# Kernel optimization log

Measured on AMD Instinct MI355X. Metric: run time of the kernel, lower is better.

The kernel has to match this reference:

```python
import jax, jax.numpy as jnp
import numpy as np

D_STATE = 16


def setup_inputs() -> dict:
    key = jax.random.key(0)
    ks = jax.random.split(key, 7)
    B, S, D = 8, 4096, 64
    ds = D_STATE
    x = jax.random.normal(ks[0], (B, S, D), dtype=jnp.float32)
    # Selection layers modeled as Linear(d_model, out). W_A scaled small so the
    # random transition matrices are contractive over 4096 steps.
    W_A = jax.random.normal(ks[1], (D, ds * ds), dtype=jnp.float32) * 0.01
    b_A = jnp.zeros((ds * ds,), dtype=jnp.float32)
    W_B = jax.random.normal(ks[2], (D, ds * D), dtype=jnp.float32) * 0.05
    b_B = jnp.zeros((ds * D,), dtype=jnp.float32)
    W_C = jax.random.normal(ks[3], (D, ds * D), dtype=jnp.float32) * 0.05
    b_C = jnp.zeros((ds * D,), dtype=jnp.float32)
    return {"x": x, "W_A": W_A, "b_A": b_A, "W_B": W_B, "b_B": b_B,
            "W_C": W_C, "b_C": b_C}


def reference(x, W_A, b_A, W_B, b_B, W_C, b_C):
    B, S, D = x.shape
    ds = D_STATE
    # Input-dependent (selective) parameters per timestep
    A = (x @ W_A + b_A).reshape(B, S, ds, ds)      # [B,S,ds,ds]
    Bm = (x @ W_B + b_B).reshape(B, S, ds, D)      # [B,S,ds,D]
    Cm = (x @ W_C + b_C).reshape(B, S, ds, D)      # [B,S,ds,D]
    # Pre-contract B_t @ x_t once: [B,S,ds]
    Bx = jnp.einsum('bsnd,bsd->bsn', Bm, x)

    def step(h, inputs):
        A_t, Bx_t = inputs                          # [B,ds,ds], [B,ds]
        h = jnp.einsum('bij,bj->bi', A_t, h) + Bx_t
        return h, h

    h0 = jnp.zeros((B, ds), dtype=x.dtype)
    _, hs = jax.lax.scan(step, h0,
                         (jnp.swapaxes(A, 0, 1), jnp.swapaxes(Bx, 0, 1)))
    hs = jnp.swapaxes(hs, 0, 1)                     # [B,S,ds]
    # output_t = C_t^T @ h_t  -> [B,S,D]
    return jnp.einsum('bsnd,bsn->bsd', Cm, hs)
```

## Files before the change

### kernel.cpp

```cpp
#include <hip/hip_runtime.h>

#define BATCH   8
#define SEQ     4096
#define DM      64
#define DS      16
#define BS      (BATCH*SEQ)
#define CHUNK   16
#define NCHT    (BS/CHUNK)
#define SG      16
#define NSG     (NCHT/SG)

typedef __attribute__((ext_vector_type(8))) __bf16 bf16x8;
typedef __attribute__((ext_vector_type(4))) float  f32x4;

__device__ __forceinline__ unsigned short f2bf(float f) {
  unsigned int u = __float_as_uint(f);
  u += 0x7fffu + ((u >> 16) & 1u);
  return (unsigned short)(u >> 16);
}
__device__ __forceinline__ float bflo(unsigned int u) { return __uint_as_float(u << 16); }
__device__ __forceinline__ float bfhi(unsigned int u) { return __uint_as_float(u & 0xffff0000u); }

#define AS_I 20
#define AS_T 324

__global__ __launch_bounds__(256) void k0_castw(
    const float* __restrict__ WA, const float* __restrict__ WB,
    const float* __restrict__ WC,
    unsigned short* __restrict__ WAt, unsigned short* __restrict__ WBt,
    unsigned short* __restrict__ WCt)
{
  const int o = blockIdx.x * 256 + threadIdx.x;
  if (o < 16384) {
    const int c = o >> 6, e = o & 63;
    WAt[o] = f2bf(WA[e * 256 + c]);
  } else if (o < 16384 + 65536) {
    const int p = o - 16384;
    const int c = p >> 6, e = p & 63;
    WBt[p] = f2bf(WB[e * 1024 + c]);
  } else {
    const int p = o - 16384 - 65536;
    const int c = p >> 6, e = p & 63;
    WCt[p] = f2bf(WC[e * 1024 + c]);
  }
}

__global__ __launch_bounds__(128) void g1(
    const float* __restrict__ x, const unsigned short* __restrict__ WBt,
    const float* __restrict__ bB, const unsigned short* __restrict__ WAt,
    const float* __restrict__ bA, unsigned short* __restrict__ xb,
    unsigned short* __restrict__ Wt_ws, float* __restrict__ u_ws,
    float* __restrict__ P_ws, float* __restrict__ v_ws)
{
  __shared__ __align__(16) unsigned char smem[32 * AS_T * 2];
  float (*xs)[68]     = (float (*)[68])smem;
  float* bBs          = (float*)(smem + 8704);
  unsigned short* As  = (unsigned short*)smem;
  __shared__ __align__(16) float bxs[32][16];
  __shared__ __align__(16) float us[2][16];

  const int tid  = threadIdx.x;
  const int lane = tid & 63;
  const int l15  = lane & 15;
  const int quad = lane >> 4;
  const int w    = tid >> 6;
  const int t0   = blockIdx.x * 32;
  const int twl  = w * 16;

  {
    const float4* xg = (const float4*)(x + (size_t)t0 * DM);
    #pragma unroll
    for (int i = 0; i < 4; ++i) {
      const int f4 = tid + 128 * i;
      ((float4*)&xs[f4 >> 4][0])[f4 & 15] = xg[f4];
    }
    ((float4*)bBs)[tid]       = ((const float4*)bB)[tid];
    ((float4*)bBs)[tid + 128] = ((const float4*)bB)[tid + 128];
    if (tid < 32) us[tid >> 4][tid & 15] = 0.f;
  }
  __syncthreads();

  bf16x8 a0, a1;
  {
    const int row = twl + l15;
    union { bf16x8 v; ushort4 s[2]; } ua, ub;
    float4 p0 = *(const float4*)&xs[row][quad * 8];
    float4 p1 = *(const float4*)&xs[row][quad * 8 + 4];
    float4 p2 = *(const float4*)&xs[row][32 + quad * 8];
    float4 p3 = *(const float4*)&xs[row][32 + quad * 8 + 4];
    ua.s[0] = (ushort4){f2bf(p0.x), f2bf(p0.y), f2bf(p0.z), f2bf(p0.w)};
    ua.s[1] = (ushort4){f2bf(p1.x), f2bf(p1.y), f2bf(p1.z), f2bf(p1.w)};
    ub.s[0] = (ushort4){f2bf(p2.x), f2bf(p2.y), f2bf(p2.z), f2bf(p2.w)};
    ub.s[1] = (ushort4){f2bf(p3.x), f2bf(p3.y), f2bf(p3.z), f2bf(p3.w)};
    a0 = ua.v; a1 = ub.v;
    unsigned short* xp = xb + (size_t)(t0 + row) * 64 + quad * 8;
    *(bf16x8*)xp        = a0;
    *(bf16x8*)(xp + 32) = a1;
  }

  #pragma unroll 2
  for (int n = 0; n < 16; ++n) {
    f32x4 ac[4];
    #pragma unroll
    for (int r = 0; r < 4; ++r) {
      const bf16x8* wv = (const bf16x8*)(WBt + (size_t)((n * 4 + r) * 16 + l15) * 64);
      f32x4 t = {0.f, 0.f, 0.f, 0.f};
      t = __builtin_amdgcn_mfma_f32_16x16x32_bf16(a0, wv[quad],     t, 0, 0, 0);
      t = __builtin_amdgcn_mfma_f32_16x16x32_bf16(a1, wv[quad + 4], t, 0, 0, 0);
      ac[r] = t;
    }
    float part[4] = {0.f, 0.f, 0.f, 0.f};
    #pragma unroll
    for (int r = 0; r < 4; ++r) {
      const float bb = bBs[n * 64 + r * 16 + l15];
      #pragma unroll
      for (int reg = 0; reg < 4; ++reg) {
        const int tl = twl + quad * 4 + reg;
        part[reg] = fmaf(ac[r][reg] + bb, xs[tl][r * 16 + l15], part[reg]);
      }
    }
    #pragma unroll
    for (int off = 1; off < 16; off <<= 1) {
      #pragma unroll
      for (int reg = 0; reg < 4; ++reg)
        part[reg] += __shfl_xor(part[reg], off, 64);
    }
    if (l15 == 0) {
      #pragma unroll
      for (int reg = 0; reg < 4; ++reg)
        bxs[twl + quad * 4 + reg][n] = part[reg];
    }
  }
  __syncthreads();

  #pragma unroll 2
  for (int ns = 0; ns < 16; ++ns) {
    const bf16x8* wv = (const bf16x8*)(WAt + (size_t)(ns * 16 + l15) * 64);
    f32x4 acc = {0.f, 0.f, 0.f, 0.f};
    acc = __builtin_amdgcn_mfma_f32_16x16x32_bf16(a0, wv[quad],     acc, 0, 0, 0);
    acc = __builtin_amdgcn_mfma_f32_16x16x32_bf16(a1, wv[quad + 4], acc, 0, 0, 0);
    const float bias = bA[ns * 16 + l15];
    #pragma unroll
    for (int r = 0; r < 4; ++r)
      As[(twl + quad * 4 + r) * AS_T + ns * AS_I + l15] = f2bf(acc[r] + bias);
  }
  __syncthreads();

  {
    bf16x8 wb;
    #pragma unroll
    for (int j = 0; j < 8; ++j) wb[j] = (__bf16)((quad * 8 + j == l15) ? 1.f : 0.f);
    f32x4 d = {0.f, 0.f, 0.f, 0.f};
    const int qq = quad & 1;

    #pragma unroll 1
    for (int t = 0; t < CHUNK; ++t) {
      const int tl = twl + t;
      const unsigned short* rp = &As[tl * AS_T + l15 * AS_I];
      uint2 r0 = *(const uint2*)(rp);
      uint2 r1 = *(const uint2*)(rp + 4);
      uint2 r2 = *(const uint2*)(rp + 8);
      uint2 r3 = *(const uint2*)(rp + 12);

      uint4 abits;
      if (quad == 0)      abits = make_uint4(r0.x, r0.y, r1.x, r1.y);
      else if (quad == 1) abits = make_uint4(r2.x, r2.y, r3.x, r3.y);
      else                abits = make_uint4(0u, 0u, 0u, 0u);
      bf16x8 af = *(bf16x8*)&abits;

      f32x4 z4 = {0.f, 0.f, 0.f, 0.f};
      d = __builtin_amdgcn_mfma_f32_16x16x32_bf16(af, wb, z4, 0, 0, 0);

      float nu = bxs[tl][l15];
      {
        float4 U0 = *(const float4*)&us[w][0];
        float4 U1 = *(const float4*)&us[w][4];
        float4 U2 = *(const float4*)&us[w][8];
        float4 U3 = *(const float4*)&us[w][12];
        nu = fmaf(bflo(r0.x), U0.x, nu); nu = fmaf(bfhi(r0.x), U0.y, nu);
        nu = fmaf(bflo(r0.y), U0.z, nu); nu = fmaf(bfhi(r0.y), U0.w, nu);
        nu = fmaf(bflo(r1.x), U1.x, nu); nu = fmaf(bfhi(r1.x), U1.y, nu);
        nu = fmaf(bflo(r1.y), U1.z, nu); nu = fmaf(bfhi(r1.y), U1.w, nu);
        nu = fmaf(bflo(r2.x), U2.x, nu); nu = fmaf(bfhi(r2.x), U2.y, nu);
        nu = fmaf(bflo(r2.y), U2.z, nu); nu = fmaf(bfhi(r2.y), U2.w, nu);
        nu = fmaf(bflo(r3.x), U3.x, nu); nu = fmaf(bfhi(r3.x), U3.y, nu);
        nu = fmaf(bflo(r3.y), U3.z, nu); nu = fmaf(bfhi(r3.y), U3.w, nu);
      }

      bf16x8 nb;
      nb[0] = (__bf16)__shfl(d[0], (2 * qq + 0) * 16 + l15, 64);
      nb[1] = (__bf16)__shfl(d[1], (2 * qq + 0) * 16 + l15, 64);
      nb[2] = (__bf16)__shfl(d[2], (2 * qq + 0) * 16 + l15, 64);
      nb[3] = (__bf16)__shfl(d[3], (2 * qq + 0) * 16 + l15, 64);
      nb[4] = (__bf16)__shfl(d[0], (2 * qq + 1) * 16 + l15, 64);
      nb[5] = (__bf16)__shfl(d[1], (2 * qq + 1) * 16 + l15, 64);
      nb[6] = (__bf16)__shfl(d[2], (2 * qq + 1) * 16 + l15, 64);
      nb[7] = (__bf16)__shfl(d[3], (2 * qq + 1) * 16 + l15, 64);
      wb = nb;

      if (quad == 0) {
        us[w][l15] = nu;
        bxs[tl][l15] = nu;
      }
      #pragma unroll
      for (int r = 0; r < 4; ++r)
        As[tl * AS_T + (quad * 4 + r) * AS_I + l15] = f2bf(d[r]);
    }

    const int chunk = blockIdx.x * 2 + w;
    #pragma unroll
    for (int r = 0; r < 4; ++r)
      P_ws[(size_t)chunk * 256 + (quad * 4 + r) * 16 + l15] = d[r];
    if (quad == 0) v_ws[(size_t)chunk * DS + l15] = us[w][l15];
  }
  __syncthreads();

  {
    uint4* Wg = (uint4*)(Wt_ws + (size_t)t0 * 256);
    #pragma unroll 1
    for (int z = 0; z < 8; ++z) {
      const int p4 = z * 128 + tid;
      const int f  = p4 * 8;
      const int t  = f >> 8, i = (f >> 4) & 15, k = f & 15;
      const unsigned short* sp = &As[t * AS_T + i * AS_I + k];
      uint2 lo = *(const uint2*)(sp);
      uint2 hi = *(const uint2*)(sp + 4);
      Wg[p4] = make_uint4(lo.x, lo.y, hi.x, hi.y);
    }
    ((float4*)(u_ws + (size_t)t0 * DS))[tid] = ((const float4*)&bxs[0][0])[tid];
  }
}

__global__ __launch_bounds__(256) void k3a(
    const float* __restrict__ P_ws, const float* __restrict__ v_ws,
    float* __restrict__ Q_ws, float* __restrict__ w_ws)
{
  __shared__ float wsv[4][16];
  const int tid  = threadIdx.x;
  const int lane = tid & 63;
  const int l15  = lane & 15;
  const int quad = lane >> 4;
  const int wv   = tid >> 6;
  const int s    = blockIdx.x * 4 + wv;
  const int qq   = quad & 1;

  if (lane < 16) wsv[wv][lane] = 0.f;
  bf16x8 wb;
  #pragma unroll
  for (int j = 0; j < 8; ++j) wb[j] = (__bf16)((quad * 8 + j == l15) ? 1.f : 0.f);
  f32x4 d = {0.f, 0.f, 0.f, 0.f};

  #pragma unroll 1
  for (int t = 0; t < SG; ++t) {
    const int chunk = s * SG + t;
    float4 p0 = {0.f,0.f,0.f,0.f}, p1 = {0.f,0.f,0.f,0.f};
    if (quad < 2) {
      const float4* pr = (const float4*)(P_ws + (size_t)chunk * 256 + l15 * 16 + quad * 8);
      p0 = pr[0]; p1 = pr[1];
    }
    bf16x8 af;
    af[0] = (__bf16)p0.x; af[1] = (__bf16)p0.y; af[2] = (__bf16)p0.z; af[3] = (__bf16)p0.w;
    af[4] = (__bf16)p1.x; af[5] = (__bf16)p1.y; af[6] = (__bf16)p1.z; af[7] = (__bf16)p1.w;

    f32x4 z4 = {0.f, 0.f, 0.f, 0.f};
    d = __builtin_amdgcn_mfma_f32_16x16x32_bf16(af, wb, z4, 0, 0, 0);

    float part = 0.f;
    if (quad < 2) {
      const float* wrow = &wsv[wv][quad * 8];
      part = p0.x*wrow[0] + p0.y*wrow[1] + p0.z*wrow[2] + p0.w*wrow[3]
           + p1.x*wrow[4] + p1.y*wrow[5] + p1.z*wrow[6] + p1.w*wrow[7];
    }
    part += __shfl_xor(part, 16, 64);
    const float nv = v_ws[(size_t)chunk * DS + l15];

    bf16x8 nb;
    nb[0] = (__bf16)__shfl(d[0], (2 * qq + 0) * 16 + l15, 64);
    nb[1] = (__bf16)__shfl(d[1], (2 * qq + 0) * 16 + l15, 64);
    nb[2] = (__bf16)__shfl(d[2], (2 * qq + 0) * 16 + l15, 64);
    nb[3] = (__bf16)__shfl(d[3], (2 * qq + 0) * 16 + l15, 64);
    nb[4] = (__bf16)__shfl(d[0], (2 * qq + 1) * 16 + l15, 64);
    nb[5] = (__bf16)__shfl(d[1], (2 * qq + 1) * 16 + l15, 64);
    nb[6] = (__bf16)__shfl(d[2], (2 * qq + 1) * 16 + l15, 64);
    nb[7] = (__bf16)__shfl(d[3], (2 * qq + 1) * 16 + l15, 64);
    wb = nb;

    if (quad == 0) wsv[wv][l15] = part + nv;
  }

  #pragma unroll
  for (int r = 0; r < 4; ++r)
    Q_ws[(size_t)s * 256 + (quad * 4 + r) * 16 + l15] = d[r];
  if (quad == 0) w_ws[(size_t)s * DS + l15] = wsv[wv][l15];
}

__global__ __launch_bounds__(128) void k3b(
    const float* __restrict__ Q_ws, const float* __restrict__ w_ws,
    float* __restrict__ hbg_ws)
{
  const int tid = threadIdx.x;
  const int b = tid >> 4;
  const int r = tid & 15;
  float h = 0.f;

  #pragma unroll 1
  for (int g = 0; g < 16; ++g) {
    const int s = b * 16 + g;
    const float4* Pr = (const float4*)&Q_ws[(size_t)s * 256 + r * 16];
    float4 c0 = Pr[0], c1 = Pr[1], c2 = Pr[2], c3 = Pr[3];
    const float vc = w_ws[(size_t)s * DS + r];
    hbg_ws[(size_t)s * DS + r] = h;
    float acc = vc;
    acc += c0.x*__shfl(h, 0,16) + c0.y*__shfl(h, 1,16) + c0.z*__shfl(h, 2,16) + c0.w*__shfl(h, 3,16);
    acc += c1.x*__shfl(h, 4,16) + c1.y*__shfl(h, 5,16) + c1.z*__shfl(h, 6,16) + c1.w*__shfl(h, 7,16);
    acc += c2.x*__shfl(h, 8,16) + c2.y*__shfl(h, 9,16) + c2.z*__shfl(h,10,16) + c2.w*__shfl(h,11,16);
    acc += c3.x*__shfl(h,12,16) + c3.y*__shfl(h,13,16) + c3.z*__shfl(h,14,16) + c3.w*__shfl(h,15,16);
    h = acc;
  }
}

__global__ __launch_bounds__(256) void k3c(
    const float* __restrict__ P_ws, const float* __restrict__ v_ws,
    const float* __restrict__ hbg_ws, float* __restrict__ hb_ws)
{
  const int tid = threadIdx.x;
  const int s = blockIdx.x * 16 + (tid >> 4);
  const int r = tid & 15;
  float h = hbg_ws[(size_t)s * DS + r];

  #pragma unroll 1
  for (int t = 0; t < SG; ++t) {
    const int chunk = s * SG + t;
    const float4* Pr = (const float4*)&P_ws[(size_t)chunk * 256 + r * 16];
    float4 c0 = Pr[0], c1 = Pr[1], c2 = Pr[2], c3 = Pr[3];
    const float vc = v_ws[(size_t)chunk * DS + r];
    hb_ws[(size_t)chunk * DS + r] = h;
    float acc = vc;
    acc += c0.x*__shfl(h, 0,16) + c0.y*__shfl(h, 1,16) + c0.z*__shfl(h, 2,16) + c0.w*__shfl(h, 3,16);
    acc += c1.x*__shfl(h, 4,16) + c1.y*__shfl(h, 5,16) + c1.z*__shfl(h, 6,16) + c1.w*__shfl(h, 7,16);
    acc += c2.x*__shfl(h, 8,16) + c2.y*__shfl(h, 9,16) + c2.z*__shfl(h,10,16) + c2.w*__shfl(h,11,16);
    acc += c3.x*__shfl(h,12,16) + c3.y*__shfl(h,13,16) + c3.z*__shfl(h,14,16) + c3.w*__shfl(h,15,16);
    h = acc;
  }
}

__global__ __launch_bounds__(256) void g2(
    const unsigned short* __restrict__ xb, const unsigned short* __restrict__ WCt,
    const float* __restrict__ bC, const unsigned short* __restrict__ Wt_ws,
    const float* __restrict__ u_ws, const float* __restrict__ hb_ws,
    float* __restrict__ out)
{
  __shared__ float hsh[64][17];
  __shared__ float bCs[1024];
  const int tid  = threadIdx.x;
  const int lane = tid & 63;
  const int l15  = lane & 15;
  const int quad = lane >> 4;
  const int w    = tid >> 6;
  const int t0   = blockIdx.x * 64;
  const int twl  = w * 16;

  ((float4*)bCs)[tid] = ((const float4*)bC)[tid];

  #pragma unroll
  for (int z = 0; z < 4; ++z) {
    const int gcell = z * 256 + tid;
    const int tl = gcell >> 4, i = gcell & 15;
    const int t = t0 + tl;
    const uint4* wr = (const uint4*)(Wt_ws + (size_t)t * 256 + i * 16);
    uint4 wa = wr[0], wbv = wr[1];
    const float4* hp = (const float4*)(hb_ws + (size_t)(t >> 4) * DS);
    float4 h0 = hp[0], h1 = hp[1], h2 = hp[2], h3 = hp[3];
    float acc = u_ws[(size_t)t * DS + i];
    acc = fmaf(bflo(wa.x),  h0.x, acc); acc = fmaf(bfhi(wa.x),  h0.y, acc);
    acc = fmaf(bflo(wa.y),  h0.z, acc); acc = fmaf(bfhi(wa.y),  h0.w, acc);
    acc = fmaf(bflo(wa.z),  h1.x, acc); acc = fmaf(bfhi(wa.z),  h1.y, acc);
    acc = fmaf(bflo(wa.w),  h1.z, acc); acc = fmaf(bfhi(wa.w),  h1.w, acc);
    acc = fmaf(bflo(wbv.x), h2.x, acc); acc = fmaf(bfhi(wbv.x), h2.y, acc);
    acc = fmaf(bflo(wbv.y), h2.z, acc); acc = fmaf(bfhi(wbv.y), h2.w, acc);
    acc = fmaf(bflo(wbv.z), h3.x, acc); acc = fmaf(bfhi(wbv.z), h3.y, acc);
    acc = fmaf(bflo(wbv.w), h3.z, acc); acc = fmaf(bfhi(wbv.w), h3.w, acc);
    hsh[tl][i] = acc;
  }

  const bf16x8* xv = (const bf16x8*)(xb + (size_t)(t0 + twl + l15) * 64);
  bf16x8 a0 = xv[quad];
  bf16x8 a1 = xv[quad + 4];
  __syncthreads();

  f32x4 ota[4];
  #pragma unroll
  for (int r = 0; r < 4; ++r) ota[r] = (f32x4){0.f, 0.f, 0.f, 0.f};

  #pragma unroll 2
  for (int n = 0; n < 16; ++n) {
    f32x4 ac[4];
    #pragma unroll
    for (int r = 0; r < 4; ++r) {
      const bf16x8* wv = (const bf16x8*)(WCt + (size_t)((n * 4 + r) * 16 + l15) * 64);
      f32x4 t = {0.f, 0.f, 0.f, 0.f};
      t = __builtin_amdgcn_mfma_f32_16x16x32_bf16(a0, wv[quad],     t, 0, 0, 0);
      t = __builtin_amdgcn_mfma_f32_16x16x32_bf16(a1, wv[quad + 4], t, 0, 0, 0);
      ac[r] = t;
    }
    float hn[4];
    #pragma unroll
    for (int reg = 0; reg < 4; ++reg) hn[reg] = hsh[twl + quad * 4 + reg][n];
    #pragma unroll
    for (int r = 0; r < 4; ++r) {
      const float bc = bCs[n * 64 + r * 16 + l15];
      #pragma unroll
      for (int reg = 0; reg < 4; ++reg)
        ota[r][reg] = fmaf(ac[r][reg] + bc, hn[reg], ota[r][reg]);
    }
  }

  #pragma unroll
  for (int r = 0; r < 4; ++r)
    #pragma unroll
    for (int reg = 0; reg < 4; ++reg)
      out[(size_t)(t0 + twl + quad * 4 + reg) * DM + r * 16 + l15] = ota[r][reg];
}

extern "C" void kernel_launch(void* const* d_in, const int* in_sizes, int n_in,
                              void* d_out, int out_size, void* d_ws, size_t ws_size,
                              hipStream_t stream) {
  const float* x  = (const float*)d_in[0];
  const float* WA = (const float*)d_in[1];
  const float* bA = (const float*)d_in[2];
  const float* WB = (const float*)d_in[3];
  const float* bB = (const float*)d_in[4];
  const float* WC = (const float*)d_in[5];
  const float* bC = (const float*)d_in[6];
  float* out = (float*)d_out;

  float* ws     = (float*)d_ws;
  float* P_ws   = ws;
  float* v_ws   = P_ws   + (size_t)NCHT * 256;
  float* u_ws   = v_ws   + (size_t)NCHT * DS;
  float* Q_ws   = u_ws   + (size_t)BS * DS;
  float* w_ws   = Q_ws   + (size_t)NSG * 256;
  float* hbg_ws = w_ws   + (size_t)NSG * DS;
  float* hb_ws  = hbg_ws + (size_t)NSG * DS;
  unsigned short* xb    = (unsigned short*)(hb_ws + (size_t)NCHT * DS);
  unsigned short* WAt   = xb  + (size_t)BS * 64;
  unsigned short* WBt   = WAt + 256 * 64;
  unsigned short* WCt   = WBt + 1024 * 64;
  unsigned short* Wt_ws = WCt + 1024 * 64;

  k0_castw<<<576,      256, 0, stream>>>(WA, WB, WC, WAt, WBt, WCt);
  g1      <<<BS / 32,  128, 0, stream>>>(x, WBt, bB, WAt, bA, xb, Wt_ws, u_ws, P_ws, v_ws);
  k3a     <<<NSG / 4,  256, 0, stream>>>(P_ws, v_ws, Q_ws, w_ws);
  k3b     <<<1,        128, 0, stream>>>(Q_ws, w_ws, hbg_ws);
  k3c     <<<NSG / 16, 256, 0, stream>>>(P_ws, v_ws, hbg_ws, hb_ws);
  g2      <<<BS / 64,  256, 0, stream>>>(xb, WCt, bC, Wt_ws, u_ws, hb_ws, out);
}
```

Measured before the change: 181.8 us.

## Enlarge g1 blocks to four waves and software-prefetch weight and A-row loads

g1 now processes 64 timesteps per 256-thread block instead of 32 per 128-thread block, with shared buffers and chunk indexing scaled to match. Weight fragments for the B, A and C projections are register double-buffered, so the next iteration's global loads are issued before the current MFMAs run. The serial in-chunk scan loop also prefetches the next timestep's A row from LDS. This aims to hide global and LDS latency behind compute. In exchange it raises register pressure, and launch_bounds(256,1) may reduce occupancy.

```diff
diff --git a/kernel.cpp b/kernel.cpp
--- a/kernel.cpp
+++ b/kernel.cpp
@@ -45,38 +45,37 @@
   }
 }
 
-__global__ __launch_bounds__(128) void g1(
+__global__ __launch_bounds__(256, 1) void g1(
     const float* __restrict__ x, const unsigned short* __restrict__ WBt,
     const float* __restrict__ bB, const unsigned short* __restrict__ WAt,
     const float* __restrict__ bA, unsigned short* __restrict__ xb,
     unsigned short* __restrict__ Wt_ws, float* __restrict__ u_ws,
     float* __restrict__ P_ws, float* __restrict__ v_ws)
 {
-  __shared__ __align__(16) unsigned char smem[32 * AS_T * 2];
+  __shared__ __align__(16) unsigned char smem[64 * AS_T * 2];
   float (*xs)[68]     = (float (*)[68])smem;
-  float* bBs          = (float*)(smem + 8704);
+  float* bBs          = (float*)(smem + 17408);
   unsigned short* As  = (unsigned short*)smem;
-  __shared__ __align__(16) float bxs[32][16];
-  __shared__ __align__(16) float us[2][16];
+  __shared__ __align__(16) float bxs[64][16];
+  __shared__ __align__(16) float us[4][16];
 
   const int tid  = threadIdx.x;
   const int lane = tid & 63;
   const int l15  = lane & 15;
   const int quad = lane >> 4;
   const int w    = tid >> 6;
-  const int t0   = blockIdx.x * 32;
+  const int t0   = blockIdx.x * 64;
   const int twl  = w * 16;
 
   {
     const float4* xg = (const float4*)(x + (size_t)t0 * DM);
     #pragma unroll
     for (int i = 0; i < 4; ++i) {
-      const int f4 = tid + 128 * i;
+      const int f4 = tid + 256 * i;
       ((float4*)&xs[f4 >> 4][0])[f4 & 15] = xg[f4];
     }
-    ((float4*)bBs)[tid]       = ((const float4*)bB)[tid];
-    ((float4*)bBs)[tid + 128] = ((const float4*)bB)[tid + 128];
-    if (tid < 32) us[tid >> 4][tid & 15] = 0.f;
+    ((float4*)bBs)[tid] = ((const float4*)bB)[tid];
+    if (tid < 64) us[tid >> 4][tid & 15] = 0.f;
   }
   __syncthreads();
 
@@ -98,51 +97,82 @@
     *(bf16x8*)(xp + 32) = a1;
   }
 
-  #pragma unroll 2
-  for (int n = 0; n < 16; ++n) {
-    f32x4 ac[4];
+  {
+    bf16x8 wf[8];
     #pragma unroll
     for (int r = 0; r < 4; ++r) {
-      const bf16x8* wv = (const bf16x8*)(WBt + (size_t)((n * 4 + r) * 16 + l15) * 64);
-      f32x4 t = {0.f, 0.f, 0.f, 0.f};
-      t = __builtin_amdgcn_mfma_f32_16x16x32_bf16(a0, wv[quad],     t, 0, 0, 0);
-      t = __builtin_amdgcn_mfma_f32_16x16x32_bf16(a1, wv[quad + 4], t, 0, 0, 0);
-      ac[r] = t;
-    }
-    float part[4] = {0.f, 0.f, 0.f, 0.f};
-    #pragma unroll
-    for (int r = 0; r < 4; ++r) {
-      const float bb = bBs[n * 64 + r * 16 + l15];
-      #pragma unroll
-      for (int reg = 0; reg < 4; ++reg) {
-        const int tl = twl + quad * 4 + reg;
-        part[reg] = fmaf(ac[r][reg] + bb, xs[tl][r * 16 + l15], part[reg]);
-      }
-    }
-    #pragma unroll
-    for (int off = 1; off < 16; off <<= 1) {
-      #pragma unroll
-      for (int reg = 0; reg < 4; ++reg)
-        part[reg] += __shfl_xor(part[reg], off, 64);
-    }
-    if (l15 == 0) {
-      #pragma unroll
-      for (int reg = 0; reg < 4; ++reg)
-        bxs[twl + quad * 4 + reg][n] = part[reg];
+      const bf16x8* wv = (const bf16x8*)(WBt + (size_t)(r * 16 + l15) * 64);
+      wf[2*r]   = wv[quad];
+      wf[2*r+1] = wv[quad + 4];
+    }
+    #pragma unroll 1
+    for (int n = 0; n < 16; ++n) {
+      bf16x8 nf[8];
+      if (n < 15) {
+        #pragma unroll
+        for (int r = 0; r < 4; ++r) {
+          const bf16x8* wv = (const bf16x8*)(WBt + (size_t)(((n+1) * 4 + r) * 16 + l15) * 64);
+          nf[2*r]   = wv[quad];
+          nf[2*r+1] = wv[quad + 4];
+        }
+      }
+      f32x4 ac[4];
+      #pragma unroll
+      for (int r = 0; r < 4; ++r) {
+        f32x4 t = {0.f, 0.f, 0.f, 0.f};
+        t = __builtin_amdgcn_mfma_f32_16x16x32_bf16(a0, wf[2*r],   t, 0, 0, 0);
+        t = __builtin_amdgcn_mfma_f32_16x16x32_bf16(a1, wf[2*r+1], t, 0, 0, 0);
+        ac[r] = t;
+      }
+      float part[4] = {0.f, 0.f, 0.f, 0.f};
+      #pragma unroll
+      for (int r = 0; r < 4; ++r) {
+        const float bb = bBs[n * 64 + r * 16 + l15];
+        #pragma unroll
+        for (int reg = 0; reg < 4; ++reg) {
+          const int tl = twl + quad * 4 + reg;
+          part[reg] = fmaf(ac[r][reg] + bb, xs[tl][r * 16 + l15], part[reg]);
+        }
+      }
+      #pragma unroll
+      for (int off = 1; off < 16; off <<= 1) {
+        #pragma unroll
+        for (int reg = 0; reg < 4; ++reg)
+          part[reg] += __shfl_xor(part[reg], off, 64);
+      }
+      if (l15 == 0) {
+        #pragma unroll
+        for (int reg = 0; reg < 4; ++reg)
+          bxs[twl + quad * 4 + reg][n] = part[reg];
+      }
+      #pragma unroll
+      for (int q = 0; q < 8; ++q) wf[q] = nf[q];
     }
   }
   __syncthreads();
 
-  #pragma unroll 2
-  for (int ns = 0; ns < 16; ++ns) {
-    const bf16x8* wv = (const bf16x8*)(WAt + (size_t)(ns * 16 + l15) * 64);
-    f32x4 acc = {0.f, 0.f, 0.f, 0.f};
-    acc = __builtin_amdgcn_mfma_f32_16x16x32_bf16(a0, wv[quad],     acc, 0, 0, 0);
-    acc = __builtin_amdgcn_mfma_f32_16x16x32_bf16(a1, wv[quad + 4], acc, 0, 0, 0);
-    const float bias = bA[ns * 16 + l15];
-    #pragma unroll
-    for (int r = 0; r < 4; ++r)
-      As[(twl + quad * 4 + r) * AS_T + ns * AS_I + l15] = f2bf(acc[r] + bias);
+  {
+    bf16x8 c0, c1;
+    {
+      const bf16x8* wv = (const bf16x8*)(WAt + (size_t)(l15) * 64);
+      c0 = wv[quad]; c1 = wv[quad + 4];
+    }
+    #pragma unroll 1
+    for (int ns = 0; ns < 16; ++ns) {
+      bf16x8 n0, n1;
+      if (ns < 15) {
+        const bf16x8* wv = (const bf16x8*)(WAt + (size_t)((ns+1) * 16 + l15) * 64);
+        n0 = wv[quad]; n1 = wv[quad + 4];
+      }
+      f32x4 acc = {0.f, 0.f, 0.f, 0.f};
+      acc = __builtin_amdgcn_mfma_f32_16x16x32_bf16(a0, c0, acc, 0, 0, 0);
+      acc = __builtin_amdgcn_mfma_f32_16x16x32_bf16(a1, c1, acc, 0, 0, 0);
+      const float bias = bA[ns * 16 + l15];
+      #pragma unroll
+      for (int r = 0; r < 4; ++r)
+        As[(twl + quad * 4 + r) * AS_T + ns * AS_I + l15] = f2bf(acc[r] + bias);
+      c0 = n0; c1 = n1;
+    }
   }
   __syncthreads();
 
@@ -153,20 +183,30 @@
     f32x4 d = {0.f, 0.f, 0.f, 0.f};
     const int qq = quad & 1;
 
+    const unsigned short* rp = &As[twl * AS_T + l15 * AS_I];
+    uint2 r0 = *(const uint2*)(rp);
+    uint2 r1 = *(const uint2*)(rp + 4);
+    uint2 r2 = *(const uint2*)(rp + 8);
+    uint2 r3 = *(const uint2*)(rp + 12);
+
     #pragma unroll 1
     for (int t = 0; t < CHUNK; ++t) {
       const int tl = twl + t;
-      const unsigned short* rp = &As[tl * AS_T + l15 * AS_I];
-      uint2 r0 = *(const uint2*)(rp);
-      uint2 r1 = *(const uint2*)(rp + 4);
-      uint2 r2 = *(const uint2*)(rp + 8);
-      uint2 r3 = *(const uint2*)(rp + 12);
 
       uint4 abits;
       if (quad == 0)      abits = make_uint4(r0.x, r0.y, r1.x, r1.y);
       else if (quad == 1) abits = make_uint4(r2.x, r2.y, r3.x, r3.y);
       else                abits = make_uint4(0u, 0u, 0u, 0u);
       bf16x8 af = *(bf16x8*)&abits;
+
+      uint2 p0, p1, p2, p3;
+      if (t < CHUNK - 1) {
+        const unsigned short* np = &As[(tl + 1) * AS_T + l15 * AS_I];
+        p0 = *(const uint2*)(np);
+        p1 = *(const uint2*)(np + 4);
+        p2 = *(const uint2*)(np + 8);
+        p3 = *(const uint2*)(np + 12);
+      }
 
       f32x4 z4 = {0.f, 0.f, 0.f, 0.f};
       d = __builtin_amdgcn_mfma_f32_16x16x32_bf16(af, wb, z4, 0, 0, 0);
@@ -205,9 +245,11 @@
       #pragma unroll
       for (int r = 0; r < 4; ++r)
         As[tl * AS_T + (quad * 4 + r) * AS_I + l15] = f2bf(d[r]);
-    }
-
-    const int chunk = blockIdx.x * 2 + w;
+
+      r0 = p0; r1 = p1; r2 = p2; r3 = p3;
+    }
+
+    const int chunk = blockIdx.x * 4 + w;
     #pragma unroll
     for (int r = 0; r < 4; ++r)
       P_ws[(size_t)chunk * 256 + (quad * 4 + r) * 16 + l15] = d[r];
@@ -219,7 +261,7 @@
     uint4* Wg = (uint4*)(Wt_ws + (size_t)t0 * 256);
     #pragma unroll 1
     for (int z = 0; z < 8; ++z) {
-      const int p4 = z * 128 + tid;
+      const int p4 = z * 256 + tid;
       const int f  = p4 * 8;
       const int t  = f >> 8, i = (f >> 4) & 15, k = f & 15;
       const unsigned short* sp = &As[t * AS_T + i * AS_I + k];
@@ -344,7 +386,7 @@
   }
 }
 
-__global__ __launch_bounds__(256) void g2(
+__global__ __launch_bounds__(256, 1) void g2(
     const unsigned short* __restrict__ xb, const unsigned short* __restrict__ WCt,
     const float* __restrict__ bC, const unsigned short* __restrict__ Wt_ws,
     const float* __restrict__ u_ws, const float* __restrict__ hb_ws,
@@ -392,26 +434,45 @@
   #pragma unroll
   for (int r = 0; r < 4; ++r) ota[r] = (f32x4){0.f, 0.f, 0.f, 0.f};
 
-  #pragma unroll 2
-  for (int n = 0; n < 16; ++n) {
-    f32x4 ac[4];
+  {
+    bf16x8 wf[8];
     #pragma unroll
     for (int r = 0; r < 4; ++r) {
-      const bf16x8* wv = (const bf16x8*)(WCt + (size_t)((n * 4 + r) * 16 + l15) * 64);
-      f32x4 t = {0.f, 0.f, 0.f, 0.f};
-      t = __builtin_amdgcn_mfma_f32_16x16x32_bf16(a0, wv[quad],     t, 0, 0, 0);
-      t = __builtin_amdgcn_mfma_f32_16x16x32_bf16(a1, wv[quad + 4], t, 0, 0, 0);
-      ac[r] = t;
-    }
-    float hn[4];
-    #pragma unroll
-    for (int reg = 0; reg < 4; ++reg) hn[reg] = hsh[twl + quad * 4 + reg][n];
-    #pragma unroll
-    for (int r = 0; r < 4; ++r) {
-      const float bc = bCs[n * 64 + r * 16 + l15];
-      #pragma unroll
-      for (int reg = 0; reg < 4; ++reg)
-        ota[r][reg] = fmaf(ac[r][reg] + bc, hn[reg], ota[r][reg]);
+      const bf16x8* wv = (const bf16x8*)(WCt + (size_t)(r * 16 + l15) * 64);
+      wf[2*r]   = wv[quad];
+      wf[2*r+1] = wv[quad + 4];
+    }
+    #pragma unroll 1
+    for (int n = 0; n < 16; ++n) {
+      bf16x8 nf[8];
+      if (n < 15) {
+        #pragma unroll
+        for (int r = 0; r < 4; ++r) {
+          const bf16x8* wv = (const bf16x8*)(WCt + (size_t)(((n+1) * 4 + r) * 16 + l15) * 64);
+          nf[2*r]   = wv[quad];
+          nf[2*r+1] = wv[quad + 4];
+        }
+      }
+      f32x4 ac[4];
+      #pragma unroll
+      for (int r = 0; r < 4; ++r) {
+        f32x4 t = {0.f, 0.f, 0.f, 0.f};
+        t = __builtin_amdgcn_mfma_f32_16x16x32_bf16(a0, wf[2*r],   t, 0, 0, 0);
+        t = __builtin_amdgcn_mfma_f32_16x16x32_bf16(a1, wf[2*r+1], t, 0, 0, 0);
+        ac[r] = t;
+      }
+      float hn[4];
+      #pragma unroll
+      for (int reg = 0; reg < 4; ++reg) hn[reg] = hsh[twl + quad * 4 + reg][n];
+      #pragma unroll
+      for (int r = 0; r < 4; ++r) {
+        const float bc = bCs[n * 64 + r * 16 + l15];
+        #pragma unroll
+        for (int reg = 0; reg < 4; ++reg)
+          ota[r][reg] = fmaf(ac[r][reg] + bc, hn[reg], ota[r][reg]);
+      }
+      #pragma unroll
+      for (int q = 0; q < 8; ++q) wf[q] = nf[q];
     }
   }
 
@@ -449,7 +510,7 @@
   unsigned short* Wt_ws = WCt + 1024 * 64;
 
   k0_castw<<<576,      256, 0, stream>>>(WA, WB, WC, WAt, WBt, WCt);
-  g1      <<<BS / 32,  128, 0, stream>>>(x, WBt, bB, WAt, bA, xb, Wt_ws, u_ws, P_ws, v_ws);
+  g1      <<<BS / 64,  256, 0, stream>>>(x, WBt, bB, WAt, bA, xb, Wt_ws, u_ws, P_ws, v_ws);
   k3a     <<<NSG / 4,  256, 0, stream>>>(P_ws, v_ws, Q_ws, w_ws);
   k3b     <<<1,        128, 0, stream>>>(Q_ws, w_ws, hbg_ws);
   k3c     <<<NSG / 16, 256, 0, stream>>>(P_ws, v_ws, hbg_ws, hb_ws);
```

After: 183.2 us. No clear change (+0.7%).
